# Performance work log

Hardware: AMD Instinct MI355X
Metric: run time of the kernel (lower is better)

Reference implementation:

```python
import jax, jax.numpy as jnp
import numpy as np

T, B, C = 2048, 8, 1024
H, K, PAD_L = 16, 31, 30
G = C // H


def setup_inputs() -> dict:
    key = jax.random.key(0)
    k1, k2 = jax.random.split(key)
    x = jax.random.normal(k1, (T, B, C), dtype=jnp.float32)
    # xavier_uniform for weight of shape (H, 1, K): fan_in=K, fan_out=H*... torch treats
    # dims as (out=H, in=1, receptive=K) -> fan_in=1*K, fan_out=H? Actually torch computes
    # fan_in = 1*K, fan_out = H*K for a (H,1,K) tensor is not right; torch: fan_in = in*rf = 1*K,
    # fan_out = out*rf = H*K? No: for (H,1,K), fan_in = 1*K, fan_out = H*K / H? Use standard formula:
    # fan_in = size(1)*K = K, fan_out = size(0)*K = H*K -> bound = sqrt(6/(K + H*K))
    bound = float(np.sqrt(6.0 / (K + H * K)))
    weight = jax.random.uniform(k2, (H, 1, K), dtype=jnp.float32, minval=-bound, maxval=bound)
    bias = jnp.zeros((C,), dtype=jnp.float32)
    return {"x": x, "weight": weight, "bias": bias}


def reference(x, weight, bias):
    # x: [T, B, C]; weight: [H, 1, K]; bias: [C]
    w = jax.nn.softmax(weight, axis=-1)  # per-head softmax over kernel taps
    # expand head weights to per-channel depthwise kernel: [C, 1, K]
    w_ch = jnp.repeat(w, G, axis=0)  # each of the G channels in head h shares w[h]
    xb = jnp.transpose(x, (1, 2, 0))  # [B, C, T]
    out = jax.lax.conv_general_dilated(
        xb, w_ch,
        window_strides=(1,),
        padding=[(PAD_L, 0)],  # left (causal) padding
        dimension_numbers=("NCH", "OIH", "NCH"),
        feature_group_count=C,
    )  # [B, C, T]
    out = jnp.transpose(out, (2, 0, 1))  # [T, B, C]
    return out + bias
```

## Files before the change

### kernel.cpp

```cpp
#include <hip/hip_runtime.h>
#include <stdint.h>

constexpr int T = 2048;
constexpr int B = 8;
constexpr int C = 1024;
constexpr int H = 16;
constexpr int K = 31;
constexpr int BC = B * C;

constexpr int TT = 32;
constexpr int NB = K - 1 + TT;
constexpr int BLOCK = 256;
constexpr int BLK_PER_CHUNK = BC / BLOCK;
constexpr int NCHUNK = T / TT;
constexpr int NBLK = BLK_PER_CHUNK * NCHUNK;

__global__ __launch_bounds__(BLOCK) void lconv_tbc_kernel(
        const float* __restrict__ x,
        const float* __restrict__ w,
        const float* __restrict__ bias,
        float* __restrict__ out) {
    const int tid = threadIdx.x;
    const int cb = blockIdx.x & (BLK_PER_CHUNK - 1);
    const int chunk = blockIdx.x / BLK_PER_CHUNK;
    const int bc = cb * BLOCK + tid;
    const int c = bc & (C - 1);
    const int h = __builtin_amdgcn_readfirstlane(c >> 6);

    const int t0 = chunk * TT;
    const float* col = x + bc;

    const float bi = bias[c];

    float buf[NB];
    if (chunk == 0) {
        #pragma unroll
        for (int j = 0; j < K - 1; ++j) buf[j] = 0.0f;
        #pragma unroll
        for (int j = K - 1; j < NB; ++j) {
            const float* a = col + (t0 + (j - (K - 1))) * BC;
            asm volatile("global_load_dword %0, %1, off"
                         : "=v"(buf[j]) : "v"(a));
        }
    } else {
        #pragma unroll
        for (int j = 0; j < NB; ++j) {
            const float* a = col + (t0 - (K - 1) + j) * BC;
            asm volatile("global_load_dword %0, %1, off"
                         : "=v"(buf[j]) : "v"(a));
        }
    }

    float tap[K];
    #pragma unroll
    for (int k = 0; k < K; ++k)
        tap[k] = __uint_as_float(__builtin_amdgcn_readfirstlane(
            __float_as_uint(w[h * K + k])));
    float m = tap[0];
    #pragma unroll
    for (int k = 1; k < K; ++k) m = fmaxf(m, tap[k]);
    float s = 0.0f;
    #pragma unroll
    for (int k = 0; k < K; ++k) s += __expf(tap[k] - m);
    const float inv = 1.0f / s;
    float wr[K];
    #pragma unroll
    for (int d = 0; d < K; ++d)
        wr[d] = __uint_as_float(__builtin_amdgcn_readfirstlane(
            __float_as_uint(__expf(tap[K - 1 - d] - m) * inv)));

    const int base = t0 * BC + bc;
    #pragma unroll
    for (int u = 0; u < TT; ++u) {
        float acc = bi;
        #pragma unroll
        for (int d = 0; d < K; ++d)
            acc = fmaf(wr[d], buf[K - 1 + u - d], acc);
        __builtin_nontemporal_store(acc, &out[base + u * BC]);
    }
}

extern "C" void kernel_launch(void* const* d_in, const int* in_sizes, int n_in,
                              void* d_out, int out_size, void* d_ws, size_t ws_size,
                              hipStream_t stream) {
    const float* x = (const float*)d_in[0];
    const float* w = (const float*)d_in[1];
    const float* bias = (const float*)d_in[2];
    float* out = (float*)d_out;

    lconv_tbc_kernel<<<dim3(NBLK), dim3(BLOCK), 0, stream>>>(x, w, bias, out);
}
```

Baseline: 28.00 us.

## Process two channels per thread with dwordx2 loads and stores

```diff
diff --git a/kernel.cpp b/kernel.cpp
--- a/kernel.cpp
+++ b/kernel.cpp
@@ -7,13 +7,16 @@
 constexpr int H = 16;
 constexpr int K = 31;
 constexpr int BC = B * C;
+constexpr int PB = BC / 2;
 
 constexpr int TT = 32;
 constexpr int NB = K - 1 + TT;
 constexpr int BLOCK = 256;
-constexpr int BLK_PER_CHUNK = BC / BLOCK;
+constexpr int NSLICE = PB / BLOCK;
 constexpr int NCHUNK = T / TT;
-constexpr int NBLK = BLK_PER_CHUNK * NCHUNK;
+constexpr int NBLK = NSLICE * NCHUNK;
+
+typedef float f32x2 __attribute__((ext_vector_type(2)));
 
 __global__ __launch_bounds__(BLOCK) void lconv_tbc_kernel(
         const float* __restrict__ x,
@@ -21,62 +24,64 @@
         const float* __restrict__ bias,
         float* __restrict__ out) {
     const int tid = threadIdx.x;
-    const int cb = blockIdx.x & (BLK_PER_CHUNK - 1);
-    const int chunk = blockIdx.x / BLK_PER_CHUNK;
-    const int bc = cb * BLOCK + tid;
-    const int c = bc & (C - 1);
-    const int h = __builtin_amdgcn_readfirstlane(c >> 6);
+    const int slice = blockIdx.x & (NSLICE - 1);
+    const int chunk = blockIdx.x / NSLICE;
+    const int p = slice * BLOCK + tid;
+    const int c = (p & 511) * 2;
+    const int h = c >> 6;
 
     const int t0 = chunk * TT;
-    const float* col = x + bc;
+    const f32x2* colp = (const f32x2*)x + p;
 
-    const float bi = bias[c];
+    const f32x2 bi = ((const f32x2*)bias)[p & 511];
 
-    float buf[NB];
+    f32x2 buf[NB];
     if (chunk == 0) {
         #pragma unroll
-        for (int j = 0; j < K - 1; ++j) buf[j] = 0.0f;
+        for (int j = 0; j < K - 1; ++j) buf[j] = (f32x2){0.f, 0.f};
         #pragma unroll
         for (int j = K - 1; j < NB; ++j) {
-            const float* a = col + (t0 + (j - (K - 1))) * BC;
-            asm volatile("global_load_dword %0, %1, off"
+            const f32x2* a = colp + (t0 + (j - (K - 1))) * PB;
+            asm volatile("global_load_dwordx2 %0, %1, off"
                          : "=v"(buf[j]) : "v"(a));
         }
     } else {
         #pragma unroll
         for (int j = 0; j < NB; ++j) {
-            const float* a = col + (t0 - (K - 1) + j) * BC;
-            asm volatile("global_load_dword %0, %1, off"
+            const f32x2* a = colp + (t0 - (K - 1) + j) * PB;
+            asm volatile("global_load_dwordx2 %0, %1, off"
                          : "=v"(buf[j]) : "v"(a));
         }
     }
 
-    float tap[K];
+    float wv[K];
     #pragma unroll
-    for (int k = 0; k < K; ++k)
-        tap[k] = __uint_as_float(__builtin_amdgcn_readfirstlane(
-            __float_as_uint(w[h * K + k])));
-    float m = tap[0];
+    for (int k = 0; k < K; ++k) wv[k] = w[h * K + k];
+    float m = wv[0];
     #pragma unroll
-    for (int k = 1; k < K; ++k) m = fmaxf(m, tap[k]);
+    for (int k = 1; k < K; ++k) m = fmaxf(m, wv[k]);
     float s = 0.0f;
     #pragma unroll
-    for (int k = 0; k < K; ++k) s += __expf(tap[k] - m);
+    for (int k = 0; k < K; ++k) {
+        wv[k] = __expf(wv[k] - m);
+        s += wv[k];
+    }
     const float inv = 1.0f / s;
     float wr[K];
     #pragma unroll
-    for (int d = 0; d < K; ++d)
-        wr[d] = __uint_as_float(__builtin_amdgcn_readfirstlane(
-            __float_as_uint(__expf(tap[K - 1 - d] - m) * inv)));
+    for (int d = 0; d < K; ++d) wr[d] = wv[K - 1 - d] * inv;
 
-    const int base = t0 * BC + bc;
+    f32x2* outp = (f32x2*)out + t0 * PB + p;
     #pragma unroll
     for (int u = 0; u < TT; ++u) {
-        float acc = bi;
+        f32x2 acc = bi;
         #pragma unroll
-        for (int d = 0; d < K; ++d)
-            acc = fmaf(wr[d], buf[K - 1 + u - d], acc);
-        __builtin_nontemporal_store(acc, &out[base + u * BC]);
+        for (int d = 0; d < K; ++d) {
+            const f32x2 v = buf[K - 1 + u - d];
+            acc.x = fmaf(wr[d], v.x, acc.x);
+            acc.y = fmaf(wr[d], v.y, acc.y);
+        }
+        outp[u * PB] = acc;
     }
 }
 
```

New measurement: 28.18 us. No clear change (+0.6%).
